# Optimization experiments

Hardware: AMD Instinct MI355X
Metric: run time of the kernel (lower is better)

Reference implementation:

```python
import jax, jax.numpy as jnp
import numpy as np

D_K = 64  # head dim used for scaling, matches init d_k


def setup_inputs() -> dict:
    key = jax.random.key(0)
    k1, k2, k3 = jax.random.split(key, 3)
    shape = (2, 2048, 16, 64)  # [batch, seq, heads, head_dim]
    q = jax.random.normal(k1, shape, dtype=jnp.float32)
    k = jax.random.normal(k2, shape, dtype=jnp.float32)
    v = jax.random.normal(k3, shape, dtype=jnp.float32)
    return {"q": q, "k": k, "v": v}


def reference(q, k, v):
    # score: [n, h, q, k]
    scale = 1.0 / np.sqrt(D_K).astype(np.float32)
    score = jnp.einsum('nqhd,nkhd->nhqk', q, k) * scale
    attn = jax.nn.softmax(score, axis=-1)
    context = jnp.einsum('nhqk,nkhd->nqhd', attn, v)
    return (context, attn)
```

## Files before the change

### kernel.cpp

```cpp
#include <hip/hip_runtime.h>

#define BATCH 2
#define SEQ   2048
#define NH    16
#define HD    64
#define RS    (NH*HD)
#define NPAIR (BATCH*NH)
#define NKT   (SEQ/64)
#define TILE_SHORTS 4096

typedef float f32x4  __attribute__((ext_vector_type(4)));
typedef short short8 __attribute__((ext_vector_type(8)));

#define GAS __attribute__((address_space(1)))
#define LAS __attribute__((address_space(3)))

__device__ __forceinline__ unsigned f2bf(float f) {
    union { float f; unsigned u; } c; c.f = f;
    return (c.u + 0x7FFFu + ((c.u >> 16) & 1u)) >> 16;
}
__device__ __forceinline__ unsigned pk(float lo, float hi) {
    return f2bf(lo) | (f2bf(hi) << 16);
}
__device__ __forceinline__ int swz(int row, int bc) {
    return (row * 128 + bc) ^ ((row & 7) << 4);
}
__device__ __forceinline__ short8 ld16(const void* p) {
    union { uint4 u; short8 s; } cv;
    cv.u = *(const uint4*)p;
    return cv.s;
}

__device__ __forceinline__ void load_qfrag(const float* Qr, int ks, short8& bq0, short8& bq1) {
    union { unsigned u[4]; short8 s; } t;
    float4 f0 = *(const float4*)(Qr + ks * 8);
    float4 f1 = *(const float4*)(Qr + ks * 8 + 4);
    t.u[0] = pk(f0.x * 0.125f, f0.y * 0.125f);
    t.u[1] = pk(f0.z * 0.125f, f0.w * 0.125f);
    t.u[2] = pk(f1.x * 0.125f, f1.y * 0.125f);
    t.u[3] = pk(f1.z * 0.125f, f1.w * 0.125f);
    bq0 = t.s;
    float4 g0 = *(const float4*)(Qr + 32 + ks * 8);
    float4 g1 = *(const float4*)(Qr + 32 + ks * 8 + 4);
    t.u[0] = pk(g0.x * 0.125f, g0.y * 0.125f);
    t.u[1] = pk(g0.z * 0.125f, g0.w * 0.125f);
    t.u[2] = pk(g1.x * 0.125f, g1.y * 0.125f);
    t.u[3] = pk(g1.z * 0.125f, g1.w * 0.125f);
    bq1 = t.s;
}

__device__ __forceinline__ void stage_k_from_f32(const float* Kt, unsigned short* Ksh, int tid) {
    #pragma unroll
    for (int i = 0; i < 2; ++i) {
        int cidx = tid + i * 256;
        int c = cidx >> 7, j = (cidx >> 6) & 1, l = cidx & 63;
        const float* src = Kt + (c * 16 + (l & 15)) * RS + j * 32 + (l >> 4) * 8;
        float4 f0 = *(const float4*)src;
        float4 f1 = *(const float4*)(src + 4);
        uint4 o = { pk(f0.x, f0.y), pk(f0.z, f0.w), pk(f1.x, f1.y), pk(f1.z, f1.w) };
        *((uint4*)Ksh + cidx) = o;
    }
}

extern "C" __global__ __launch_bounds__(256)
void pack_kv(const float* __restrict__ k, const float* __restrict__ v,
             unsigned short* __restrict__ ktl, unsigned short* __restrict__ vtl)
{
    __shared__ float Vf[64 * 65];
    const int bid = blockIdx.x;
    const int tid = threadIdx.x;

    if (bid < NPAIR * NKT) {
        const int kti = bid & 31, h = (bid >> 5) & 15, n = bid >> 9;
        const float* Kg = k + (((long)n * SEQ + kti * 64) * NH + h) * HD;
        stage_k_from_f32(Kg, ktl + (long)bid * TILE_SHORTS, tid);
    } else {
        const int b2 = bid - NPAIR * NKT;
        const int kti = b2 & 31, h = (b2 >> 5) & 15, n = b2 >> 9;
        const float* Vg = v + (((long)n * SEQ + kti * 64) * NH + h) * HD;
        #pragma unroll
        for (int i = 0; i < 4; ++i) {
            int idx = tid + i * 256;
            int row = idx >> 4, c4 = idx & 15;
            float4 f = *(const float4*)(Vg + row * RS + c4 * 4);
            Vf[row * 65 + c4 * 4 + 0] = f.x;
            Vf[row * 65 + c4 * 4 + 1] = f.y;
            Vf[row * 65 + c4 * 4 + 2] = f.z;
            Vf[row * 65 + c4 * 4 + 3] = f.w;
        }
        __syncthreads();
        uint4* out = (uint4*)(vtl + (long)b2 * TILE_SHORTS);
        #pragma unroll
        for (int i = 0; i < 2; ++i) {
            int cidx = tid + i * 256;
            int c = cidx >> 7, j = (cidx >> 6) & 1, l = cidx & 63;
            int d = c * 16 + (l & 15);
            int kb = j * 32 + (l >> 4) * 8;
            float a0 = Vf[(kb + 0) * 65 + d], a1 = Vf[(kb + 1) * 65 + d];
            float a2 = Vf[(kb + 2) * 65 + d], a3 = Vf[(kb + 3) * 65 + d];
            float a4 = Vf[(kb + 4) * 65 + d], a5 = Vf[(kb + 5) * 65 + d];
            float a6 = Vf[(kb + 6) * 65 + d], a7 = Vf[(kb + 7) * 65 + d];
            uint4 o = { pk(a0, a1), pk(a2, a3), pk(a4, a5), pk(a6, a7) };
            out[cidx] = o;
        }
    }
}

extern "C" __global__ __launch_bounds__(256, 4)
void sdpa_kernel(const float* __restrict__ q,
                 const unsigned short* __restrict__ ktl,
                 const unsigned short* __restrict__ vtl,
                 float* __restrict__ ctx, float* __restrict__ attn,
                 float* __restrict__ linv_out, int skip_pair)
{
    __shared__ unsigned short SM[4][TILE_SHORTS];
    __shared__ unsigned short Ps[4][1024];

    const int bid0 = blockIdx.x;
    const int bid  = ((bid0 & 7) << 7) | (bid0 >> 3);
    const int qt = bid & 31, pair = bid >> 5;
    const int h = pair & 15, n = pair >> 4;
    const int tid = threadIdx.x;
    const int w = tid >> 6, lane = tid & 63, lh = lane & 15, ks = lane >> 4;
    const bool wattn = (pair != skip_pair);

    const float* Qr = q + (((long)n * SEQ + qt * 64 + w * 16 + lh) * NH + h) * HD;
    short8 bq0, bq1;
    load_qfrag(Qr, ks, bq0, bq1);

    const unsigned short* Ktile = ktl + (long)pair * NKT * TILE_SHORTS;
    const unsigned short* Vtile = vtl + (long)pair * NKT * TILE_SHORTS;

    auto stage = [&](unsigned short* lbuf, const unsigned short* gt) {
        #pragma unroll
        for (int i = 0; i < 2; ++i) {
            const unsigned short* g = gt + w * 1024 + i * 512 + lane * 8;
            unsigned short* l = lbuf + w * 1024 + i * 512;
            __builtin_amdgcn_global_load_lds((const GAS unsigned int*)g,
                                             (LAS unsigned int*)l, 16, 0, 0);
        }
    };

    stage(SM[0], Ktile);
    stage(SM[1], Ktile + TILE_SHORTS);
    float lsum = 0.f;
    for (int kt = 0; kt < NKT; ++kt) {
        if (kt + 2 < NKT) {
            stage(SM[(kt + 2) & 3], Ktile + (long)(kt + 2) * TILE_SHORTS);
            asm volatile("s_waitcnt vmcnt(4)" ::: "memory");
        } else if (kt + 1 < NKT) {
            asm volatile("s_waitcnt vmcnt(2)" ::: "memory");
        } else {
            asm volatile("s_waitcnt vmcnt(0)" ::: "memory");
        }
        __builtin_amdgcn_s_barrier();
        const char* Kb = (const char*)SM[kt & 3];
        #pragma unroll
        for (int c = 0; c < 4; ++c) {
            short8 a0 = ld16(Kb + ((c * 2 + 0) * 64 + lane) * 16);
            short8 a1 = ld16(Kb + ((c * 2 + 1) * 64 + lane) * 16);
            f32x4 z = {0.f, 0.f, 0.f, 0.f};
            z = __builtin_amdgcn_mfma_f32_16x16x32_bf16(a0, bq0, z, 0, 0, 0);
            z = __builtin_amdgcn_mfma_f32_16x16x32_bf16(a1, bq1, z, 0, 0, 0);
            lsum += __expf(z[0]) + __expf(z[1]) + __expf(z[2]) + __expf(z[3]);
        }
    }
    lsum += __shfl_xor(lsum, 16);
    lsum += __shfl_xor(lsum, 32);
    const float linv = 1.0f / lsum;
    const float nml2 = -__log2f(lsum);

    if (pair == skip_pair && linv_out && ks == 0) {
        linv_out[qt * 64 + w * 16 + lh] = linv;
    }

    f32x4 oacc[4];
    #pragma unroll
    for (int cd = 0; cd < 4; ++cd) oacc[cd] = (f32x4){0.f, 0.f, 0.f, 0.f};

    float* attnW = attn + (((long)pair) * SEQ + qt * 64 + w * 16 + lh) * SEQ + ks * 4;
    char* Pw = (char*)Ps[w];

    stage(SM[0], Ktile);
    stage(SM[2], Vtile);
    asm volatile("s_waitcnt vmcnt(0)" ::: "memory");
    __builtin_amdgcn_s_barrier();

    for (int kt = 0; kt < NKT; ++kt) {
        const int cur = kt & 1;
        if (kt < NKT - 1) {
            stage(SM[cur ^ 1], Ktile + (long)(kt + 1) * TILE_SHORTS);
            stage(SM[2 + (cur ^ 1)], Vtile + (long)(kt + 1) * TILE_SHORTS);
        }
        asm volatile("" ::: "memory");

        const char* Kb = (const char*)SM[cur];
        f32x4 s[4];
        #pragma unroll
        for (int c = 0; c < 4; ++c) {
            short8 a0 = ld16(Kb + ((c * 2 + 0) * 64 + lane) * 16);
            short8 a1 = ld16(Kb + ((c * 2 + 1) * 64 + lane) * 16);
            f32x4 z = {0.f, 0.f, 0.f, 0.f};
            z = __builtin_amdgcn_mfma_f32_16x16x32_bf16(a0, bq0, z, 0, 0, 0);
            z = __builtin_amdgcn_mfma_f32_16x16x32_bf16(a1, bq1, z, 0, 0, 0);
            s[c] = z;
        }
        #pragma unroll
        for (int c = 0; c < 4; ++c) {
            f32x4 pv;
            #pragma unroll
            for (int r = 0; r < 4; ++r)
                pv[r] = __builtin_amdgcn_exp2f(fmaf(s[c][r], 1.44269504f, nml2));
            if (wattn) *(f32x4*)(attnW + (long)kt * 64 + c * 16) = pv;
            unsigned r0, r1;
            asm("v_cvt_pk_bf16_f32 %0, %1, %2" : "=v"(r0) : "v"(pv[0]), "v"(pv[1]));
            asm("v_cvt_pk_bf16_f32 %0, %1, %2" : "=v"(r1) : "v"(pv[2]), "v"(pv[3]));
            uint2 u2 = { r0, r1 };
            *(uint2*)(Pw + swz(lh, c * 32 + ks * 8)) = u2;
        }
        short8 pa0 = ld16(Pw + swz(lh, ks * 16));
        short8 pa1 = ld16(Pw + swz(lh, 64 + ks * 16));
        const char* Vb = (const char*)SM[2 + cur];
        #pragma unroll
        for (int cd = 0; cd < 4; ++cd) {
            short8 bv0 = ld16(Vb + ((cd * 2 + 0) * 64 + lane) * 16);
            short8 bv1 = ld16(Vb + ((cd * 2 + 1) * 64 + lane) * 16);
            oacc[cd] = __builtin_amdgcn_mfma_f32_16x16x32_bf16(pa0, bv0, oacc[cd], 0, 0, 0);
            oacc[cd] = __builtin_amdgcn_mfma_f32_16x16x32_bf16(pa1, bv1, oacc[cd], 0, 0, 0);
        }
        if (kt < NKT - 1) {
            if (wattn) asm volatile("s_waitcnt vmcnt(4)" ::: "memory");
            else       asm volatile("s_waitcnt vmcnt(0)" ::: "memory");
            __builtin_amdgcn_s_barrier();
        }
    }

    float* ctxW = ctx + (((long)n * SEQ + qt * 64 + w * 16 + ks * 4) * NH + h) * HD + lh;
    #pragma unroll
    for (int cd = 0; cd < 4; ++cd) {
        #pragma unroll
        for (int r = 0; r < 4; ++r) {
            ctxW[r * RS + cd * 16] = oacc[cd][r];
        }
    }
}

extern "C" __global__ __launch_bounds__(256)
void attn_fill_fast(const float* __restrict__ q, const float* __restrict__ k,
                    float* __restrict__ attn, const float* __restrict__ linv_in,
                    int pair)
{
    __shared__ unsigned short Ksh[TILE_SHORTS];
    const int n = pair >> 4, h = pair & 15;
    const int qt = blockIdx.x & 31, kt = blockIdx.x >> 5;
    const int tid = threadIdx.x;
    const int w = tid >> 6, lane = tid & 63, lh = lane & 15, ks = lane >> 4;

    const float* Qr = q + (((long)n * SEQ + qt * 64 + w * 16 + lh) * NH + h) * HD;
    short8 bq0, bq1;
    load_qfrag(Qr, ks, bq0, bq1);
    const float linv = linv_in[qt * 64 + w * 16 + lh];

    const float* Kt = k + (((long)n * SEQ + kt * 64) * NH + h) * HD;
    stage_k_from_f32(Kt, Ksh, tid);
    __syncthreads();

    float* attnW = attn + (((long)pair) * SEQ + qt * 64 + w * 16 + lh) * SEQ + ks * 4;
    #pragma unroll
    for (int c = 0; c < 4; ++c) {
        short8 a0 = ld16((const char*)Ksh + ((c * 2 + 0) * 64 + lane) * 16);
        short8 a1 = ld16((const char*)Ksh + ((c * 2 + 1) * 64 + lane) * 16);
        f32x4 z = {0.f, 0.f, 0.f, 0.f};
        z = __builtin_amdgcn_mfma_f32_16x16x32_bf16(a0, bq0, z, 0, 0, 0);
        z = __builtin_amdgcn_mfma_f32_16x16x32_bf16(a1, bq1, z, 0, 0, 0);
        f32x4 pv;
        pv[0] = __expf(z[0]) * linv;
        pv[1] = __expf(z[1]) * linv;
        pv[2] = __expf(z[2]) * linv;
        pv[3] = __expf(z[3]) * linv;
        *(f32x4*)(attnW + (long)kt * 64 + c * 16) = pv;
    }
}

extern "C" __global__ __launch_bounds__(256, 4)
void attn_fill_slow(const float* __restrict__ q, const float* __restrict__ k,
                    float* __restrict__ attn, int pair)
{
    __shared__ unsigned short Ksh[TILE_SHORTS];
    const int n = pair >> 4, h = pair & 15;
    const int qt = blockIdx.x;
    const int tid = threadIdx.x;
    const int w = tid >> 6, lane = tid & 63, lh = lane & 15, ks = lane >> 4;

    const float* Qr = q + (((long)n * SEQ + qt * 64 + w * 16 + lh) * NH + h) * HD;
    short8 bq0, bq1;
    load_qfrag(Qr, ks, bq0, bq1);

    const float* Kg = k + ((long)n * SEQ * NH + h) * HD;

    float lsum = 0.f;
    for (int kt = 0; kt < NKT; ++kt) {
        __syncthreads();
        stage_k_from_f32(Kg + (long)kt * 64 * RS, Ksh, tid);
        __syncthreads();
        #pragma unroll
        for (int c = 0; c < 4; ++c) {
            short8 a0 = ld16((const char*)Ksh + ((c * 2 + 0) * 64 + lane) * 16);
            short8 a1 = ld16((const char*)Ksh + ((c * 2 + 1) * 64 + lane) * 16);
            f32x4 z = {0.f, 0.f, 0.f, 0.f};
            z = __builtin_amdgcn_mfma_f32_16x16x32_bf16(a0, bq0, z, 0, 0, 0);
            z = __builtin_amdgcn_mfma_f32_16x16x32_bf16(a1, bq1, z, 0, 0, 0);
            lsum += __expf(z[0]) + __expf(z[1]) + __expf(z[2]) + __expf(z[3]);
        }
    }
    lsum += __shfl_xor(lsum, 16);
    lsum += __shfl_xor(lsum, 32);
    const float linv = 1.0f / lsum;

    float* attnW = attn + (((long)pair) * SEQ + qt * 64 + w * 16 + lh) * SEQ + ks * 4;
    for (int kt = 0; kt < NKT; ++kt) {
        __syncthreads();
        stage_k_from_f32(Kg + (long)kt * 64 * RS, Ksh, tid);
        __syncthreads();
        #pragma unroll
        for (int c = 0; c < 4; ++c) {
            short8 a0 = ld16((const char*)Ksh + ((c * 2 + 0) * 64 + lane) * 16);
            short8 a1 = ld16((const char*)Ksh + ((c * 2 + 1) * 64 + lane) * 16);
            f32x4 z = {0.f, 0.f, 0.f, 0.f};
            z = __builtin_amdgcn_mfma_f32_16x16x32_bf16(a0, bq0, z, 0, 0, 0);
            z = __builtin_amdgcn_mfma_f32_16x16x32_bf16(a1, bq1, z, 0, 0, 0);
            f32x4 pv;
            pv[0] = __expf(z[0]) * linv;
            pv[1] = __expf(z[1]) * linv;
            pv[2] = __expf(z[2]) * linv;
            pv[3] = __expf(z[3]) * linv;
            *(f32x4*)(attnW + (long)kt * 64 + c * 16) = pv;
        }
    }
}

extern "C" void kernel_launch(void* const* d_in, const int* in_sizes, int n_in,
                              void* d_out, int out_size, void* d_ws, size_t ws_size,
                              hipStream_t stream)
{
    const float* q = (const float*)d_in[0];
    const float* k = (const float*)d_in[1];
    const float* v = (const float*)d_in[2];
    float* ctx  = (float*)d_out;
    float* attn = ctx + (size_t)BATCH * SEQ * NH * HD;

    const size_t tiles_shorts = (size_t)NPAIR * NKT * TILE_SHORTS;
    const size_t ws_need = 2 * tiles_shorts * sizeof(unsigned short);

    unsigned short *ktl, *vtl;
    int skip;
    if (ws_size >= ws_need) {
        ktl = (unsigned short*)d_ws;
        vtl = ktl + tiles_shorts;
        skip = -1;
    } else {
        ktl = (unsigned short*)(attn + (size_t)(NPAIR - 1) * SEQ * SEQ);
        vtl = ktl + tiles_shorts;
        skip = NPAIR - 1;
    }

    const bool linv_fits = (ws_size >= SEQ * sizeof(float));
    float* linv_ws = (skip >= 0 && linv_fits) ? (float*)d_ws : nullptr;

    hipLaunchKernelGGL(pack_kv, dim3(2 * NPAIR * NKT), dim3(256), 0, stream, k, v, ktl, vtl);
    hipLaunchKernelGGL(sdpa_kernel, dim3(NPAIR * NKT), dim3(256), 0, stream,
                       q, ktl, vtl, ctx, attn, linv_ws, skip);
    if (skip >= 0) {
        if (linv_ws) {
            hipLaunchKernelGGL(attn_fill_fast, dim3(NKT * 32), dim3(256), 0, stream,
                               q, k, attn, linv_ws, skip);
        } else {
            hipLaunchKernelGGL(attn_fill_slow, dim3(32), dim3(256), 0, stream, q, k, attn, skip);
        }
    }
}
```

Before: 187.7 us.

## Split softmax row-sum pass across waves by key tile, reducing via LDS

The first pass computing the softmax denominator is restructured so that each wave loads all four query fragments and handles a quarter of the key tiles, reading K directly from global memory instead of staging it through LDS with barriers. Partial sums per query row are reduced across waves through shared memory. The aim is to remove the per-tile barrier and LDS staging overhead and reuse each K load across four query fragments. In exchange it adds register pressure from eight Q fragments and four accumulators, and performs uncoalesced-style direct global loads without prefetch.

```diff
diff --git a/kernel.cpp b/kernel.cpp
--- a/kernel.cpp
+++ b/kernel.cpp
@@ -124,12 +124,15 @@
     const int w = tid >> 6, lane = tid & 63, lh = lane & 15, ks = lane >> 4;
     const bool wattn = (pair != skip_pair);
 
-    const float* Qr = q + (((long)n * SEQ + qt * 64 + w * 16 + lh) * NH + h) * HD;
-    short8 bq0, bq1;
-    load_qfrag(Qr, ks, bq0, bq1);
-
     const unsigned short* Ktile = ktl + (long)pair * NKT * TILE_SHORTS;
     const unsigned short* Vtile = vtl + (long)pair * NKT * TILE_SHORTS;
+
+    short8 qf[8];
+    #pragma unroll
+    for (int f = 0; f < 4; ++f) {
+        const float* Qf = q + (((long)n * SEQ + qt * 64 + f * 16 + lh) * NH + h) * HD;
+        load_qfrag(Qf, ks, qf[2 * f], qf[2 * f + 1]);
+    }
 
     auto stage = [&](unsigned short* lbuf, const unsigned short* gt) {
         #pragma unroll
@@ -141,38 +144,49 @@
         }
     };
 
-    stage(SM[0], Ktile);
-    stage(SM[1], Ktile + TILE_SHORTS);
-    float lsum = 0.f;
-    for (int kt = 0; kt < NKT; ++kt) {
-        if (kt + 2 < NKT) {
-            stage(SM[(kt + 2) & 3], Ktile + (long)(kt + 2) * TILE_SHORTS);
-            asm volatile("s_waitcnt vmcnt(4)" ::: "memory");
-        } else if (kt + 1 < NKT) {
-            asm volatile("s_waitcnt vmcnt(2)" ::: "memory");
-        } else {
-            asm volatile("s_waitcnt vmcnt(0)" ::: "memory");
-        }
-        __builtin_amdgcn_s_barrier();
-        const char* Kb = (const char*)SM[kt & 3];
-        #pragma unroll
-        for (int c = 0; c < 4; ++c) {
-            short8 a0 = ld16(Kb + ((c * 2 + 0) * 64 + lane) * 16);
-            short8 a1 = ld16(Kb + ((c * 2 + 1) * 64 + lane) * 16);
-            f32x4 z = {0.f, 0.f, 0.f, 0.f};
-            z = __builtin_amdgcn_mfma_f32_16x16x32_bf16(a0, bq0, z, 0, 0, 0);
-            z = __builtin_amdgcn_mfma_f32_16x16x32_bf16(a1, bq1, z, 0, 0, 0);
-            lsum += __expf(z[0]) + __expf(z[1]) + __expf(z[2]) + __expf(z[3]);
-        }
-    }
-    lsum += __shfl_xor(lsum, 16);
-    lsum += __shfl_xor(lsum, 32);
+    f32x4 sums[4];
+    #pragma unroll
+    for (int f = 0; f < 4; ++f) sums[f] = (f32x4){0.f, 0.f, 0.f, 0.f};
+
+    for (int t = 0; t < 8; ++t) {
+        const int kt = w + t * 4;
+        const char* T = (const char*)(Ktile + (long)kt * TILE_SHORTS);
+        #pragma unroll
+        for (int c = 0; c < 4; ++c) {
+            short8 a0 = ld16(T + ((c * 2 + 0) * 64 + lane) * 16);
+            short8 a1 = ld16(T + ((c * 2 + 1) * 64 + lane) * 16);
+            #pragma unroll
+            for (int f = 0; f < 4; ++f) {
+                f32x4 z = {0.f, 0.f, 0.f, 0.f};
+                z = __builtin_amdgcn_mfma_f32_16x16x32_bf16(a0, qf[2 * f], z, 0, 0, 0);
+                z = __builtin_amdgcn_mfma_f32_16x16x32_bf16(a1, qf[2 * f + 1], z, 0, 0, 0);
+                sums[f][0] += __expf(z[0]);
+                sums[f][1] += __expf(z[1]);
+                sums[f][2] += __expf(z[2]);
+                sums[f][3] += __expf(z[3]);
+            }
+        }
+    }
+    float* Lred = (float*)Ps;
+    #pragma unroll
+    for (int f = 0; f < 4; ++f) {
+        float tsum = sums[f][0] + sums[f][1] + sums[f][2] + sums[f][3];
+        tsum += __shfl_xor(tsum, 16);
+        tsum += __shfl_xor(tsum, 32);
+        if (lane < 16) Lred[w * 64 + f * 16 + lane] = tsum;
+    }
+    __syncthreads();
+    const int myq = w * 16 + lh;
+    const float lsum = Lred[0 * 64 + myq] + Lred[1 * 64 + myq]
+                     + Lred[2 * 64 + myq] + Lred[3 * 64 + myq];
     const float linv = 1.0f / lsum;
     const float nml2 = -__log2f(lsum);
 
     if (pair == skip_pair && linv_out && ks == 0) {
-        linv_out[qt * 64 + w * 16 + lh] = linv;
-    }
+        linv_out[qt * 64 + myq] = linv;
+    }
+
+    const short8 bq0 = qf[2 * w], bq1 = qf[2 * w + 1];
 
     f32x4 oacc[4];
     #pragma unroll
```

Result: slower. 352.7 us (+87.9%).

## Split attention kernel into separate row-sum and output passes

Applied to the files above, without the earlier changes.

Splits the fused kernel into two launches. The first computes softmax row sums over K and writes them to a workspace buffer; the second reads them, then computes the normalized attention and the context. Workspace layout changes to store per-row sums. This may let each kernel use registers and LDS better, but adds a launch and a global round trip. In the no-workspace fallback, the sums buffer sits in the attn tail, which attn_fill_slow later overwrites.

```diff
diff --git a/kernel.cpp b/kernel.cpp
--- a/kernel.cpp
+++ b/kernel.cpp
@@ -8,6 +8,7 @@
 #define NPAIR (BATCH*NH)
 #define NKT   (SEQ/64)
 #define TILE_SHORTS 4096
+#define LSUM_FLOATS (NPAIR*NKT*64)
 
 typedef float f32x4  __attribute__((ext_vector_type(4)));
 typedef short short8 __attribute__((ext_vector_type(8)));
@@ -107,14 +108,11 @@
 }
 
 extern "C" __global__ __launch_bounds__(256, 4)
-void sdpa_kernel(const float* __restrict__ q,
-                 const unsigned short* __restrict__ ktl,
-                 const unsigned short* __restrict__ vtl,
-                 float* __restrict__ ctx, float* __restrict__ attn,
-                 float* __restrict__ linv_out, int skip_pair)
+void sdpa_pass1(const float* __restrict__ q,
+                const unsigned short* __restrict__ ktl,
+                float* __restrict__ lsum_out)
 {
     __shared__ unsigned short SM[4][TILE_SHORTS];
-    __shared__ unsigned short Ps[4][1024];
 
     const int bid0 = blockIdx.x;
     const int bid  = ((bid0 & 7) << 7) | (bid0 >> 3);
@@ -122,14 +120,12 @@
     const int h = pair & 15, n = pair >> 4;
     const int tid = threadIdx.x;
     const int w = tid >> 6, lane = tid & 63, lh = lane & 15, ks = lane >> 4;
-    const bool wattn = (pair != skip_pair);
 
     const float* Qr = q + (((long)n * SEQ + qt * 64 + w * 16 + lh) * NH + h) * HD;
     short8 bq0, bq1;
     load_qfrag(Qr, ks, bq0, bq1);
 
     const unsigned short* Ktile = ktl + (long)pair * NKT * TILE_SHORTS;
-    const unsigned short* Vtile = vtl + (long)pair * NKT * TILE_SHORTS;
 
     auto stage = [&](unsigned short* lbuf, const unsigned short* gt) {
         #pragma unroll
@@ -167,12 +163,48 @@
     }
     lsum += __shfl_xor(lsum, 16);
     lsum += __shfl_xor(lsum, 32);
-    const float linv = 1.0f / lsum;
+
+    if (ks == 0) lsum_out[bid * 64 + w * 16 + lh] = lsum;
+}
+
+extern "C" __global__ __launch_bounds__(256, 4)
+void sdpa_pass2(const float* __restrict__ q,
+                const unsigned short* __restrict__ ktl,
+                const unsigned short* __restrict__ vtl,
+                const float* __restrict__ lsum_in,
+                float* __restrict__ ctx, float* __restrict__ attn,
+                int skip_pair)
+{
+    __shared__ unsigned short SM[4][TILE_SHORTS];
+    __shared__ unsigned short Ps[4][1024];
+
+    const int bid0 = blockIdx.x;
+    const int bid  = ((bid0 & 7) << 7) | (bid0 >> 3);
+    const int qt = bid & 31, pair = bid >> 5;
+    const int h = pair & 15, n = pair >> 4;
+    const int tid = threadIdx.x;
+    const int w = tid >> 6, lane = tid & 63, lh = lane & 15, ks = lane >> 4;
+    const bool wattn = (pair != skip_pair);
+
+    const float* Qr = q + (((long)n * SEQ + qt * 64 + w * 16 + lh) * NH + h) * HD;
+    short8 bq0, bq1;
+    load_qfrag(Qr, ks, bq0, bq1);
+
+    const float lsum = lsum_in[bid * 64 + w * 16 + lh];
     const float nml2 = -__log2f(lsum);
 
-    if (pair == skip_pair && linv_out && ks == 0) {
-        linv_out[qt * 64 + w * 16 + lh] = linv;
-    }
+    const unsigned short* Ktile = ktl + (long)pair * NKT * TILE_SHORTS;
+    const unsigned short* Vtile = vtl + (long)pair * NKT * TILE_SHORTS;
+
+    auto stage = [&](unsigned short* lbuf, const unsigned short* gt) {
+        #pragma unroll
+        for (int i = 0; i < 2; ++i) {
+            const unsigned short* g = gt + w * 1024 + i * 512 + lane * 8;
+            unsigned short* l = lbuf + w * 1024 + i * 512;
+            __builtin_amdgcn_global_load_lds((const GAS unsigned int*)g,
+                                             (LAS unsigned int*)l, 16, 0, 0);
+        }
+    };
 
     f32x4 oacc[4];
     #pragma unroll
@@ -247,7 +279,7 @@
 
 extern "C" __global__ __launch_bounds__(256)
 void attn_fill_fast(const float* __restrict__ q, const float* __restrict__ k,
-                    float* __restrict__ attn, const float* __restrict__ linv_in,
+                    float* __restrict__ attn, const float* __restrict__ lsum_in,
                     int pair)
 {
     __shared__ unsigned short Ksh[TILE_SHORTS];
@@ -259,7 +291,7 @@
     const float* Qr = q + (((long)n * SEQ + qt * 64 + w * 16 + lh) * NH + h) * HD;
     short8 bq0, bq1;
     load_qfrag(Qr, ks, bq0, bq1);
-    const float linv = linv_in[qt * 64 + w * 16 + lh];
+    const float linv = 1.0f / lsum_in[(pair * 32 + qt) * 64 + w * 16 + lh];
 
     const float* Kt = k + (((long)n * SEQ + kt * 64) * NH + h) * HD;
     stage_k_from_f32(Kt, Ksh, tid);
@@ -349,31 +381,40 @@
     float* ctx  = (float*)d_out;
     float* attn = ctx + (size_t)BATCH * SEQ * NH * HD;
 
+    const size_t lsum_bytes   = LSUM_FLOATS * sizeof(float);
     const size_t tiles_shorts = (size_t)NPAIR * NKT * TILE_SHORTS;
-    const size_t ws_need = 2 * tiles_shorts * sizeof(unsigned short);
-
+    const size_t tiles_bytes  = 2 * tiles_shorts * sizeof(unsigned short);
+
+    float* lsum_buf;
     unsigned short *ktl, *vtl;
     int skip;
-    if (ws_size >= ws_need) {
-        ktl = (unsigned short*)d_ws;
+
+    if (ws_size >= lsum_bytes + tiles_bytes) {
+        lsum_buf = (float*)d_ws;
+        ktl = (unsigned short*)((char*)d_ws + lsum_bytes);
         vtl = ktl + tiles_shorts;
         skip = -1;
-    } else {
+    } else if (ws_size >= lsum_bytes) {
+        lsum_buf = (float*)d_ws;
         ktl = (unsigned short*)(attn + (size_t)(NPAIR - 1) * SEQ * SEQ);
         vtl = ktl + tiles_shorts;
         skip = NPAIR - 1;
-    }
-
-    const bool linv_fits = (ws_size >= SEQ * sizeof(float));
-    float* linv_ws = (skip >= 0 && linv_fits) ? (float*)d_ws : nullptr;
+    } else {
+        char* tail = (char*)(attn + (size_t)(NPAIR - 1) * SEQ * SEQ);
+        lsum_buf = (float*)tail;
+        ktl = (unsigned short*)(tail + lsum_bytes);
+        vtl = ktl + tiles_shorts;
+        skip = NPAIR - 1;
+    }
 
     hipLaunchKernelGGL(pack_kv, dim3(2 * NPAIR * NKT), dim3(256), 0, stream, k, v, ktl, vtl);
-    hipLaunchKernelGGL(sdpa_kernel, dim3(NPAIR * NKT), dim3(256), 0, stream,
-                       q, ktl, vtl, ctx, attn, linv_ws, skip);
+    hipLaunchKernelGGL(sdpa_pass1, dim3(NPAIR * NKT), dim3(256), 0, stream, q, ktl, lsum_buf);
+    hipLaunchKernelGGL(sdpa_pass2, dim3(NPAIR * NKT), dim3(256), 0, stream,
+                       q, ktl, vtl, lsum_buf, ctx, attn, skip);
     if (skip >= 0) {
-        if (linv_ws) {
+        if (ws_size >= lsum_bytes) {
             hipLaunchKernelGGL(attn_fill_fast, dim3(NKT * 32), dim3(256), 0, stream,
-                               q, k, attn, linv_ws, skip);
+                               q, k, attn, lsum_buf, skip);
         } else {
             hipLaunchKernelGGL(attn_fill_slow, dim3(32), dim3(256), 0, stream, q, k, attn, skip);
         }
```

Result: slower. 201.8 us (+7.5%).
